# Performance work log

Hardware: AMD Instinct MI355X
Metric: run time of the kernel (lower is better)

The kernel has to match this reference:

```python
import jax, jax.numpy as jnp
from jax import lax
import numpy as np

INPUT_DIMS = 512
HIDDEN_DIMS = 1024
OUTPUT_DIMS = 512
BATCH = 64
T = 256


def setup_inputs() -> dict:
    key = jax.random.key(0)
    ks = jax.random.split(key, 9)
    s_ih = 1.0 / np.sqrt(HIDDEN_DIMS)
    inp = {
        "x": jax.random.normal(ks[0], (BATCH, INPUT_DIMS, T), dtype=jnp.float32),
        # LSTMCell params (PyTorch gate order: i, f, g, o)
        "W_ih": jax.random.uniform(ks[1], (4 * HIDDEN_DIMS, INPUT_DIMS), minval=-s_ih, maxval=s_ih, dtype=jnp.float32),
        "W_hh": jax.random.uniform(ks[2], (4 * HIDDEN_DIMS, HIDDEN_DIMS), minval=-s_ih, maxval=s_ih, dtype=jnp.float32),
        "b_ih": jax.random.uniform(ks[3], (4 * HIDDEN_DIMS,), minval=-s_ih, maxval=s_ih, dtype=jnp.float32),
        "b_hh": jax.random.uniform(ks[4], (4 * HIDDEN_DIMS,), minval=-s_ih, maxval=s_ih, dtype=jnp.float32),
        # Output linear
        "W_out": jax.random.uniform(ks[5], (OUTPUT_DIMS, HIDDEN_DIMS), minval=-s_ih, maxval=s_ih, dtype=jnp.float32),
        "b_out": jax.random.uniform(ks[6], (OUTPUT_DIMS,), minval=-s_ih, maxval=s_ih, dtype=jnp.float32),
        # Initial state (learned-ish constants in the original, sampled from randn)
        "h0": jax.random.normal(ks[7], (1, HIDDEN_DIMS), dtype=jnp.float32),
        "c0": jax.random.normal(ks[8], (1, HIDDEN_DIMS), dtype=jnp.float32),
    }
    return inp


def reference(x, W_ih, W_hh, b_ih, b_hh, W_out, b_out, h0, c0):
    B, I, Tlen = x.shape
    H = W_hh.shape[1]
    h = jnp.broadcast_to(h0, (B, H))
    c = jnp.broadcast_to(c0, (B, H))
    xs = jnp.transpose(x, (2, 0, 1))  # [T, B, I]
    # Precompute the input projection for all timesteps in one GEMM.
    x_proj = jnp.einsum("tbi,gi->tbg", xs, W_ih) + b_ih  # [T, B, 4H]

    def step(carry, xp):
        h, c = carry
        gates = xp + h @ W_hh.T + b_hh  # [B, 4H]
        i_g, f_g, g_g, o_g = jnp.split(gates, 4, axis=-1)
        i_g = jax.nn.sigmoid(i_g)
        f_g = jax.nn.sigmoid(f_g)
        g_g = jnp.tanh(g_g)
        o_g = jax.nn.sigmoid(o_g)
        c_new = f_g * c + i_g * g_g
        h_new = o_g * jnp.tanh(c_new)
        # NOTE: original applies the output head to the CELL state c, not h.
        p = jax.nn.softmax(c_new @ W_out.T + b_out, axis=1)  # [B, O]
        return (h_new, c_new), p

    _, ps = lax.scan(step, (h, c), x_proj)  # ps: [T, B, O]
    # torch.cat along dim 0 per timestep == stack then flatten first two dims.
    return ps.reshape(Tlen * B, -1)
```

## Files before the change

kernel.cpp:

```cpp
#include <hip/hip_runtime.h>


#define T_ 256

typedef __attribute__((ext_vector_type(8))) short bf16x8;
typedef __attribute__((ext_vector_type(4))) float floatx4;
typedef __attribute__((ext_vector_type(4))) int intx4;

__device__ __forceinline__ unsigned short f2bf(float f) {
  unsigned u = __builtin_bit_cast(unsigned, f);
  u += 0x7FFFu + ((u >> 16) & 1u);
  return (unsigned short)(u >> 16);
}

__device__ __forceinline__ float sigm(float x) { return 1.0f / (1.0f + __expf(-x)); }

__global__ void cvt_w(const float* __restrict__ w, unsigned short* __restrict__ o) {
  const size_t g = (size_t)blockIdx.x * 256 + threadIdx.x;
  const float* s = w + g * 8;
  bf16x8 v;
#pragma unroll
  for (int i = 0; i < 8; ++i) v[i] = (short)f2bf(s[i]);
  *(bf16x8*)(o + g * 8) = v;
}

__global__ void transpose_x(const float* __restrict__ x, unsigned short* __restrict__ xT) {
  __shared__ float tile[32][33];
  const int b = blockIdx.z, i0 = blockIdx.y * 32, t0 = blockIdx.x * 32;
  const int tx = threadIdx.x & 31, ty = threadIdx.x >> 5;
#pragma unroll
  for (int p = 0; p < 4; ++p) {
    const int i = ty + p * 8;
    tile[i][tx] = x[((size_t)b * 512 + i0 + i) * 256 + t0 + tx];
  }
  __syncthreads();
#pragma unroll
  for (int p = 0; p < 4; ++p) {
    const int t = ty + p * 8;
    xT[((size_t)(t0 + t) * 64 + b) * 512 + i0 + tx] = f2bf(tile[tx][t]);
  }
}

__global__ __launch_bounds__(512, 1) void lstm_rec(
    const float* __restrict__ Whh, const float* __restrict__ Wih,
    const float* __restrict__ bih, const float* __restrict__ bhh,
    const float* __restrict__ h0, const float* __restrict__ c0,
    const unsigned short* __restrict__ xT,
    unsigned short* __restrict__ hbuf,
    unsigned short* __restrict__ call,
    unsigned* __restrict__ flags)
{
  const int tid = threadIdx.x;
  const int lane = tid & 63;
  const int wv = tid >> 6;
  const int nh = wv & 1, kq = wv >> 1;
  const int mg = blockIdx.x & 3, ng = blockIdx.x >> 2;
  const int l15 = lane & 15, lq = lane >> 4;
  const int row = mg * 16 + l15;

  unsigned* grpflags = flags + mg * 64;
  unsigned* myflag   = grpflags + ng;

  __shared__ unsigned short hlds[16 * 1032];
  __shared__ float gpart[4][16][66];

  bf16x8 bfrag[2][12];
#pragma unroll
  for (int nt = 0; nt < 2; ++nt) {
    const int ncol = (2 * nh + nt) * 1024 + ng * 16 + l15;
#pragma unroll
    for (int ks = 0; ks < 12; ++ks) {
      const int kg = kq * 384 + ks * 32 + lq * 8;
      const float* s = (kg < 1024) ? (Whh + (size_t)ncol * 1024 + kg)
                                   : (Wih + (size_t)ncol * 512 + (kg - 1024));
      bf16x8 v;
#pragma unroll
      for (int i = 0; i < 8; ++i) v[i] = (short)f2bf(s[i]);
      bfrag[nt][ks] = v;
    }
  }

  const int m_loc = tid >> 4, j = tid & 15;
  const int row_g = mg * 16 + m_loc;
  const int unit = ng * 16 + j;
  float c_reg = 0.f, bs0 = 0.f, bs1 = 0.f, bs2 = 0.f, bs3 = 0.f;
  if (tid < 256) {
    c_reg = c0[unit];
    bs0 = bih[unit] + bhh[unit];
    bs1 = bih[1024 + unit] + bhh[1024 + unit];
    bs2 = bih[2048 + unit] + bhh[2048 + unit];
    bs3 = bih[3072 + unit] + bhh[3072 + unit];
    unsigned short* hp = hbuf + 65536 + row_g * 1024 + unit;
    const unsigned hv = f2bf(h0[unit]);
    asm volatile("global_store_short %0, %1, off sc0 sc1"
                 :: "v"(hp), "v"(hv) : "memory");
    asm volatile("s_waitcnt vmcnt(0)" ::: "memory");
  }
  __syncthreads();
  if (tid == 0)
    __hip_atomic_store(myflag, 1u, __ATOMIC_RELAXED, __HIP_MEMORY_SCOPE_SYSTEM);

  for (int t = 0; t < T_; ++t) {
    const unsigned short* bx = xT + ((size_t)t * 64 + row) * 512;
    floatx4 zero = {0.f, 0.f, 0.f, 0.f};
    floatx4 acc0 = zero, acc1 = zero;

#pragma unroll
    for (int ks = 0; ks < 12; ++ks) {
      const int kg = kq * 384 + ks * 32 + lq * 8;
      if (kg >= 1024) {
        const bf16x8 af = *(const bf16x8*)(bx + (kg - 1024));
        acc0 = __builtin_amdgcn_mfma_f32_16x16x32_bf16(af, bfrag[0][ks], acc0, 0, 0, 0);
        acc1 = __builtin_amdgcn_mfma_f32_16x16x32_bf16(af, bfrag[1][ks], acc1, 0, 0, 0);
      }
    }

    if (wv == 0) {
      const unsigned tgt = (unsigned)(t + 1);
      while (!__all(__hip_atomic_load(grpflags + lane, __ATOMIC_RELAXED,
                                      __HIP_MEMORY_SCOPE_SYSTEM) >= tgt)) {}
    }
    __syncthreads();

    {
      const unsigned short* hprev = hbuf + ((t + 1) & 1) * 65536;
      const unsigned short* gsrc = hprev + (size_t)(mg * 16) * 1024 + (size_t)tid * 8;
      intx4 a0, a1, a2, a3;
      asm volatile(
          "global_load_dwordx4 %0, %4, off sc0 sc1\n\t"
          "global_load_dwordx4 %1, %5, off sc0 sc1\n\t"
          "global_load_dwordx4 %2, %6, off sc0 sc1\n\t"
          "global_load_dwordx4 %3, %7, off sc0 sc1\n\t"
          "s_waitcnt vmcnt(0)"
          : "=v"(a0), "=v"(a1), "=v"(a2), "=v"(a3)
          : "v"(gsrc), "v"(gsrc + 4096), "v"(gsrc + 8192), "v"(gsrc + 12288)
          : "memory");
      intx4 av[4] = {a0, a1, a2, a3};
#pragma unroll
      for (int p = 0; p < 4; ++p) {
        const int e = tid + p * 512;
        const int r = e >> 7, col = (e & 127) * 8;
        *(intx4*)(hlds + r * 1032 + col) = av[p];
      }
    }
    __syncthreads();

#pragma unroll
    for (int ks = 0; ks < 12; ++ks) {
      const int kg = kq * 384 + ks * 32 + lq * 8;
      if (kg < 1024) {
        const bf16x8 af = *(const bf16x8*)(hlds + l15 * 1032 + kg);
        acc0 = __builtin_amdgcn_mfma_f32_16x16x32_bf16(af, bfrag[0][ks], acc0, 0, 0, 0);
        acc1 = __builtin_amdgcn_mfma_f32_16x16x32_bf16(af, bfrag[1][ks], acc1, 0, 0, 0);
      }
    }

#pragma unroll
    for (int r = 0; r < 4; ++r) {
      gpart[kq][lq * 4 + r][(2 * nh) * 16 + l15]     = acc0[r];
      gpart[kq][lq * 4 + r][(2 * nh + 1) * 16 + l15] = acc1[r];
    }
    __syncthreads();

    if (tid < 256) {
      float gi = bs0, gf = bs1, gg = bs2, go = bs3;
#pragma unroll
      for (int q = 0; q < 4; ++q) {
        gi += gpart[q][m_loc][j];
        gf += gpart[q][m_loc][16 + j];
        gg += gpart[q][m_loc][32 + j];
        go += gpart[q][m_loc][48 + j];
      }
      const float iv = sigm(gi), fv = sigm(gf), gv = tanhf(gg), ov = sigm(go);
      c_reg = fv * c_reg + iv * gv;
      const float hv = ov * tanhf(c_reg);
      call[((size_t)t * 64 + row_g) * 1024 + unit] = f2bf(c_reg);
      unsigned short* hp = hbuf + (t & 1) * 65536 + row_g * 1024 + unit;
      const unsigned hb = f2bf(hv);
      asm volatile("global_store_short %0, %1, off sc0 sc1"
                   :: "v"(hp), "v"(hb) : "memory");
      asm volatile("s_waitcnt vmcnt(0)" ::: "memory");
    }
    __syncthreads();
    if (tid == 0)
      __hip_atomic_store(myflag, (unsigned)(t + 2), __ATOMIC_RELAXED,
                         __HIP_MEMORY_SCOPE_SYSTEM);
  }
}

__global__ __launch_bounds__(256, 1) void lstm_head(
    const unsigned short* __restrict__ call,
    const unsigned short* __restrict__ wout,
    const float* __restrict__ bout,
    float* __restrict__ out)
{
  const int tb = blockIdx.x;
  const int lane = threadIdx.x & 63;
  const int wv = threadIdx.x >> 6;
  const int l15 = lane & 15, lq = lane >> 4;

  __shared__ float sred[2][4][64];

  floatx4 zero = {0.f, 0.f, 0.f, 0.f};
  floatx4 acc[4][8];
#pragma unroll
  for (int mt = 0; mt < 4; ++mt)
#pragma unroll
    for (int nt = 0; nt < 8; ++nt) acc[mt][nt] = zero;

  const unsigned short* abase = call + ((size_t)tb * 64 + l15) * 1024 + lq * 8;
  const unsigned short* bbase = wout + ((size_t)(wv * 128 + l15)) * 1024 + lq * 8;

#pragma unroll 2
  for (int ks = 0; ks < 32; ++ks) {
    bf16x8 a[4];
#pragma unroll
    for (int mt = 0; mt < 4; ++mt)
      a[mt] = *(const bf16x8*)(abase + (size_t)mt * 16 * 1024 + ks * 32);
#pragma unroll
    for (int nt = 0; nt < 8; ++nt) {
      const bf16x8 b = *(const bf16x8*)(bbase + (size_t)nt * 16 * 1024 + ks * 32);
#pragma unroll
      for (int mt = 0; mt < 4; ++mt)
        acc[mt][nt] = __builtin_amdgcn_mfma_f32_16x16x32_bf16(a[mt], b, acc[mt][nt], 0, 0, 0);
    }
  }

#pragma unroll
  for (int nt = 0; nt < 8; ++nt) {
    const float bo = bout[wv * 128 + nt * 16 + l15];
#pragma unroll
    for (int mt = 0; mt < 4; ++mt)
#pragma unroll
      for (int r = 0; r < 4; ++r) acc[mt][nt][r] += bo;
  }

  float rmax[4][4];
#pragma unroll
  for (int mt = 0; mt < 4; ++mt)
#pragma unroll
    for (int r = 0; r < 4; ++r) {
      float m = acc[mt][0][r];
#pragma unroll
      for (int nt = 1; nt < 8; ++nt) m = fmaxf(m, acc[mt][nt][r]);
      m = fmaxf(m, __shfl_xor(m, 1, 64));
      m = fmaxf(m, __shfl_xor(m, 2, 64));
      m = fmaxf(m, __shfl_xor(m, 4, 64));
      m = fmaxf(m, __shfl_xor(m, 8, 64));
      rmax[mt][r] = m;
    }
  if (l15 == 0) {
#pragma unroll
    for (int mt = 0; mt < 4; ++mt)
#pragma unroll
      for (int r = 0; r < 4; ++r) sred[0][wv][mt * 16 + lq * 4 + r] = rmax[mt][r];
  }
  __syncthreads();
  float gmax[4][4], rsum[4][4];
#pragma unroll
  for (int mt = 0; mt < 4; ++mt)
#pragma unroll
    for (int r = 0; r < 4; ++r) {
      const int rw = mt * 16 + lq * 4 + r;
      gmax[mt][r] = fmaxf(fmaxf(sred[0][0][rw], sred[0][1][rw]),
                          fmaxf(sred[0][2][rw], sred[0][3][rw]));
      rsum[mt][r] = 0.f;
    }
#pragma unroll
  for (int mt = 0; mt < 4; ++mt)
#pragma unroll
    for (int nt = 0; nt < 8; ++nt)
#pragma unroll
      for (int r = 0; r < 4; ++r) {
        const float e = __expf(acc[mt][nt][r] - gmax[mt][r]);
        acc[mt][nt][r] = e;
        rsum[mt][r] += e;
      }
#pragma unroll
  for (int mt = 0; mt < 4; ++mt)
#pragma unroll
    for (int r = 0; r < 4; ++r) {
      float s = rsum[mt][r];
      s += __shfl_xor(s, 1, 64);
      s += __shfl_xor(s, 2, 64);
      s += __shfl_xor(s, 4, 64);
      s += __shfl_xor(s, 8, 64);
      rsum[mt][r] = s;
    }
  if (l15 == 0) {
#pragma unroll
    for (int mt = 0; mt < 4; ++mt)
#pragma unroll
      for (int r = 0; r < 4; ++r) sred[1][wv][mt * 16 + lq * 4 + r] = rsum[mt][r];
  }
  __syncthreads();
#pragma unroll
  for (int mt = 0; mt < 4; ++mt)
#pragma unroll
    for (int r = 0; r < 4; ++r) {
      const int rw = mt * 16 + lq * 4 + r;
      const float inv = 1.0f / (sred[1][0][rw] + sred[1][1][rw] +
                                sred[1][2][rw] + sred[1][3][rw]);
      float* orow = out + ((size_t)tb * 64 + rw) * 512 + wv * 128 + l15;
#pragma unroll
      for (int nt = 0; nt < 8; ++nt) orow[nt * 16] = acc[mt][nt][r] * inv;
    }
}

extern "C" void kernel_launch(void* const* d_in, const int* in_sizes, int n_in,
                              void* d_out, int out_size, void* d_ws, size_t ws_size,
                              hipStream_t stream) {
  const float* x    = (const float*)d_in[0];
  const float* Wih  = (const float*)d_in[1];
  const float* Whh  = (const float*)d_in[2];
  const float* bih  = (const float*)d_in[3];
  const float* bhh  = (const float*)d_in[4];
  const float* Wout = (const float*)d_in[5];
  const float* bout = (const float*)d_in[6];
  const float* h0   = (const float*)d_in[7];
  const float* c0   = (const float*)d_in[8];
  float* out = (float*)d_out;

  char* ws = (char*)d_ws;
  unsigned* flags       = (unsigned*)(ws + 0);
  unsigned short* hbuf  = (unsigned short*)(ws + 4096);
  unsigned short* woutb = (unsigned short*)(ws + 266240);
  unsigned short* xT    = (unsigned short*)(ws + 1314816);
  unsigned short* call  = (unsigned short*)(ws + 18092032);

  hipMemsetAsync(flags, 0, 1024, stream);
  cvt_w<<<256, 256, 0, stream>>>(Wout, woutb);
  transpose_x<<<dim3(8, 16, 64), 256, 0, stream>>>(x, xT);
  lstm_rec<<<256, 512, 0, stream>>>(Whh, Wih, bih, bhh, h0, c0, xT, hbuf, call, flags);
  lstm_head<<<256, 256, 0, stream>>>(call, woutb, bout, out);
}
```

Before: 1.479 ms.

## Restructure LSTM recurrence sync: LDS token spin, counter-based flag publish, direct h loads

The recurrent kernel now splits the K dimension across all 8 waves, each covering all four gates, and loads h fragments straight from global memory into registers instead of staging them through LDS. The per-step barriers around polling and flag publishing are replaced by an LDS token that wave 0 sets after a vectorized flag poll, and by an LDS atomic counter so the last finishing wave publishes the step flag. Partial sums go into a double-buffered transposed LDS array, so only one __syncthreads remains per step. The goal is to shorten the serial per-timestep critical path, but correctness now depends on subtle memory-ordering assumptions between waves and the reduction reads twice as many partial sums.

Result: slower. 1.899 ms (+28.3%).

```diff
diff --git a/kernel.cpp b/kernel.cpp
--- a/kernel.cpp
+++ b/kernel.cpp
@@ -6,6 +6,7 @@
 typedef __attribute__((ext_vector_type(8))) short bf16x8;
 typedef __attribute__((ext_vector_type(4))) float floatx4;
 typedef __attribute__((ext_vector_type(4))) int intx4;
+typedef __attribute__((ext_vector_type(4))) unsigned uintx4;
 
 __device__ __forceinline__ unsigned short f2bf(float f) {
   unsigned u = __builtin_bit_cast(unsigned, f);
@@ -41,7 +42,7 @@
   }
 }
 
-__global__ __launch_bounds__(512, 1) void lstm_rec(
+__global__ __launch_bounds__(512, 2) void lstm_rec(
     const float* __restrict__ Whh, const float* __restrict__ Wih,
     const float* __restrict__ bih, const float* __restrict__ bhh,
     const float* __restrict__ h0, const float* __restrict__ c0,
@@ -52,31 +53,32 @@
 {
   const int tid = threadIdx.x;
   const int lane = tid & 63;
-  const int wv = tid >> 6;
-  const int nh = wv & 1, kq = wv >> 1;
+  const int w = tid >> 6;
   const int mg = blockIdx.x & 3, ng = blockIdx.x >> 2;
   const int l15 = lane & 15, lq = lane >> 4;
   const int row = mg * 16 + l15;
 
   unsigned* grpflags = flags + mg * 64;
   unsigned* myflag   = grpflags + ng;
-
-  __shared__ unsigned short hlds[16 * 1032];
-  __shared__ float gpart[4][16][66];
-
-  bf16x8 bfrag[2][12];
-#pragma unroll
-  for (int nt = 0; nt < 2; ++nt) {
-    const int ncol = (2 * nh + nt) * 1024 + ng * 16 + l15;
-#pragma unroll
-    for (int ks = 0; ks < 12; ++ks) {
-      const int kg = kq * 384 + ks * 32 + lq * 8;
-      const float* s = (kg < 1024) ? (Whh + (size_t)ncol * 1024 + kg)
-                                   : (Wih + (size_t)ncol * 512 + (kg - 1024));
+  const unsigned* pollp = grpflags + (lane & 15) * 4;
+
+  __shared__ float gpartT[2][8][64][17];
+  __shared__ unsigned token;
+  __shared__ unsigned scnt;
+
+  bf16x8 bfrag[4][6];
+#pragma unroll
+  for (int g = 0; g < 4; ++g) {
+    const int ncol = g * 1024 + ng * 16 + l15;
+#pragma unroll
+    for (int i = 0; i < 6; ++i) {
+      const int gk = w + 8 * i;
+      const float* s = (gk < 32) ? (Whh + (size_t)ncol * 1024 + gk * 32 + lq * 8)
+                                 : (Wih + (size_t)ncol * 512 + (gk - 32) * 32 + lq * 8);
       bf16x8 v;
 #pragma unroll
-      for (int i = 0; i < 8; ++i) v[i] = (short)f2bf(s[i]);
-      bfrag[nt][ks] = v;
+      for (int e = 0; e < 8; ++e) v[e] = (short)f2bf(s[e]);
+      bfrag[g][i] = v;
     }
   }
 
@@ -84,6 +86,10 @@
   const int row_g = mg * 16 + m_loc;
   const int unit = ng * 16 + j;
   float c_reg = 0.f, bs0 = 0.f, bs1 = 0.f, bs2 = 0.f, bs3 = 0.f;
+
+  if (tid == 0) { token = 0u; scnt = 0u; }
+  __syncthreads();
+
   if (tid < 256) {
     c_reg = c0[unit];
     bs0 = bih[unit] + bhh[unit];
@@ -92,84 +98,81 @@
     bs3 = bih[3072 + unit] + bhh[3072 + unit];
     unsigned short* hp = hbuf + 65536 + row_g * 1024 + unit;
     const unsigned hv = f2bf(h0[unit]);
-    asm volatile("global_store_short %0, %1, off sc0 sc1"
-                 :: "v"(hp), "v"(hv) : "memory");
-    asm volatile("s_waitcnt vmcnt(0)" ::: "memory");
-  }
-  __syncthreads();
-  if (tid == 0)
-    __hip_atomic_store(myflag, 1u, __ATOMIC_RELAXED, __HIP_MEMORY_SCOPE_SYSTEM);
+    asm volatile("global_store_short %0, %1, off sc0 sc1\n\t"
+                 "s_waitcnt vmcnt(0)" :: "v"(hp), "v"(hv) : "memory");
+    if (lane == 0) {
+      const unsigned old = atomicAdd(&scnt, 1u);
+      if (old == 3u) {
+        const unsigned one = 1u;
+        asm volatile("global_store_dword %0, %1, off sc0 sc1"
+                     :: "v"(myflag), "v"(one) : "memory");
+      }
+    }
+  }
 
   for (int t = 0; t < T_; ++t) {
-    const unsigned short* bx = xT + ((size_t)t * 64 + row) * 512;
+    const unsigned short* bx = xT + ((size_t)t * 64 + row) * 512 + lq * 8;
+    intx4 x4, x5;
+    asm volatile("global_load_dwordx4 %0, %2, off\n\t"
+                 "global_load_dwordx4 %1, %3, off"
+                 : "=v"(x4), "=v"(x5)
+                 : "v"(bx + w * 32), "v"(bx + (w + 8) * 32) : "memory");
+
+    const unsigned tgt = (unsigned)(t + 1);
+    if (w == 0) {
+      uintx4 f;
+      do {
+        asm volatile("global_load_dwordx4 %0, %1, off sc0 sc1\n\t"
+                     "s_waitcnt vmcnt(0)"
+                     : "=v"(f) : "v"(pollp) : "memory");
+      } while (!__all(f[0] >= tgt && f[1] >= tgt && f[2] >= tgt && f[3] >= tgt));
+      __hip_atomic_store(&token, tgt, __ATOMIC_RELAXED, __HIP_MEMORY_SCOPE_WORKGROUP);
+    } else {
+      while (__hip_atomic_load(&token, __ATOMIC_RELAXED,
+                               __HIP_MEMORY_SCOPE_WORKGROUP) < tgt) {}
+    }
+
+    const unsigned short* bh = hbuf + ((t + 1) & 1) * 65536 + (size_t)row * 1024 + lq * 8;
+    intx4 h0v, h1v, h2v, h3v;
+    asm volatile(
+        "global_load_dwordx4 %0, %4, off sc0 sc1\n\t"
+        "global_load_dwordx4 %1, %5, off sc0 sc1\n\t"
+        "global_load_dwordx4 %2, %6, off sc0 sc1\n\t"
+        "global_load_dwordx4 %3, %7, off sc0 sc1\n\t"
+        "s_waitcnt vmcnt(0)"
+        : "=v"(h0v), "=v"(h1v), "=v"(h2v), "=v"(h3v)
+        : "v"(bh + w * 32), "v"(bh + (w + 8) * 32),
+          "v"(bh + (w + 16) * 32), "v"(bh + (w + 24) * 32) : "memory");
+
+    bf16x8 a[6];
+    a[0] = __builtin_bit_cast(bf16x8, h0v);
+    a[1] = __builtin_bit_cast(bf16x8, h1v);
+    a[2] = __builtin_bit_cast(bf16x8, h2v);
+    a[3] = __builtin_bit_cast(bf16x8, h3v);
+    a[4] = __builtin_bit_cast(bf16x8, x4);
+    a[5] = __builtin_bit_cast(bf16x8, x5);
+
     floatx4 zero = {0.f, 0.f, 0.f, 0.f};
-    floatx4 acc0 = zero, acc1 = zero;
-
-#pragma unroll
-    for (int ks = 0; ks < 12; ++ks) {
-      const int kg = kq * 384 + ks * 32 + lq * 8;
-      if (kg >= 1024) {
-        const bf16x8 af = *(const bf16x8*)(bx + (kg - 1024));
-        acc0 = __builtin_amdgcn_mfma_f32_16x16x32_bf16(af, bfrag[0][ks], acc0, 0, 0, 0);
-        acc1 = __builtin_amdgcn_mfma_f32_16x16x32_bf16(af, bfrag[1][ks], acc1, 0, 0, 0);
-      }
-    }
-
-    if (wv == 0) {
-      const unsigned tgt = (unsigned)(t + 1);
-      while (!__all(__hip_atomic_load(grpflags + lane, __ATOMIC_RELAXED,
-                                      __HIP_MEMORY_SCOPE_SYSTEM) >= tgt)) {}
-    }
-    __syncthreads();
-
-    {
-      const unsigned short* hprev = hbuf + ((t + 1) & 1) * 65536;
-      const unsigned short* gsrc = hprev + (size_t)(mg * 16) * 1024 + (size_t)tid * 8;
-      intx4 a0, a1, a2, a3;
-      asm volatile(
-          "global_load_dwordx4 %0, %4, off sc0 sc1\n\t"
-          "global_load_dwordx4 %1, %5, off sc0 sc1\n\t"
-          "global_load_dwordx4 %2, %6, off sc0 sc1\n\t"
-          "global_load_dwordx4 %3, %7, off sc0 sc1\n\t"
-          "s_waitcnt vmcnt(0)"
-          : "=v"(a0), "=v"(a1), "=v"(a2), "=v"(a3)
-          : "v"(gsrc), "v"(gsrc + 4096), "v"(gsrc + 8192), "v"(gsrc + 12288)
-          : "memory");
-      intx4 av[4] = {a0, a1, a2, a3};
-#pragma unroll
-      for (int p = 0; p < 4; ++p) {
-        const int e = tid + p * 512;
-        const int r = e >> 7, col = (e & 127) * 8;
-        *(intx4*)(hlds + r * 1032 + col) = av[p];
-      }
-    }
-    __syncthreads();
-
-#pragma unroll
-    for (int ks = 0; ks < 12; ++ks) {
-      const int kg = kq * 384 + ks * 32 + lq * 8;
-      if (kg < 1024) {
-        const bf16x8 af = *(const bf16x8*)(hlds + l15 * 1032 + kg);
-        acc0 = __builtin_amdgcn_mfma_f32_16x16x32_bf16(af, bfrag[0][ks], acc0, 0, 0, 0);
-        acc1 = __builtin_amdgcn_mfma_f32_16x16x32_bf16(af, bfrag[1][ks], acc1, 0, 0, 0);
-      }
-    }
-
-#pragma unroll
-    for (int r = 0; r < 4; ++r) {
-      gpart[kq][lq * 4 + r][(2 * nh) * 16 + l15]     = acc0[r];
-      gpart[kq][lq * 4 + r][(2 * nh + 1) * 16 + l15] = acc1[r];
-    }
+    floatx4 acc[4] = {zero, zero, zero, zero};
+#pragma unroll
+    for (int i = 0; i < 6; ++i)
+#pragma unroll
+      for (int g = 0; g < 4; ++g)
+        acc[g] = __builtin_amdgcn_mfma_f32_16x16x32_bf16(a[i], bfrag[g][i], acc[g], 0, 0, 0);
+
+#pragma unroll
+    for (int g = 0; g < 4; ++g)
+      *(floatx4*)&gpartT[t & 1][w][g * 16 + l15][lq * 4] = acc[g];
     __syncthreads();
 
     if (tid < 256) {
       float gi = bs0, gf = bs1, gg = bs2, go = bs3;
 #pragma unroll
-      for (int q = 0; q < 4; ++q) {
-        gi += gpart[q][m_loc][j];
-        gf += gpart[q][m_loc][16 + j];
-        gg += gpart[q][m_loc][32 + j];
-        go += gpart[q][m_loc][48 + j];
+      for (int q = 0; q < 8; ++q) {
+        gi += gpartT[t & 1][q][j][m_loc];
+        gf += gpartT[t & 1][q][16 + j][m_loc];
+        gg += gpartT[t & 1][q][32 + j][m_loc];
+        go += gpartT[t & 1][q][48 + j][m_loc];
       }
       const float iv = sigm(gi), fv = sigm(gf), gv = tanhf(gg), ov = sigm(go);
       c_reg = fv * c_reg + iv * gv;
@@ -177,14 +180,17 @@
       call[((size_t)t * 64 + row_g) * 1024 + unit] = f2bf(c_reg);
       unsigned short* hp = hbuf + (t & 1) * 65536 + row_g * 1024 + unit;
       const unsigned hb = f2bf(hv);
-      asm volatile("global_store_short %0, %1, off sc0 sc1"
-                   :: "v"(hp), "v"(hb) : "memory");
-      asm volatile("s_waitcnt vmcnt(0)" ::: "memory");
-    }
-    __syncthreads();
-    if (tid == 0)
-      __hip_atomic_store(myflag, (unsigned)(t + 2), __ATOMIC_RELAXED,
-                         __HIP_MEMORY_SCOPE_SYSTEM);
+      asm volatile("global_store_short %0, %1, off sc0 sc1\n\t"
+                   "s_waitcnt vmcnt(0)" :: "v"(hp), "v"(hb) : "memory");
+      if (lane == 0) {
+        const unsigned old = atomicAdd(&scnt, 1u);
+        if (old == (unsigned)(4 * t + 7)) {
+          const unsigned val = (unsigned)(t + 2);
+          asm volatile("global_store_dword %0, %1, off sc0 sc1"
+                       :: "v"(myflag), "v"(val) : "memory");
+        }
+      }
+    }
   }
 }
 
```
